# Optimization experiments

Measured on AMD Instinct MI355X. Metric: run time of the kernel, lower is better.

The kernel has to match this reference:

```python
import jax, jax.numpy as jnp
import numpy as np

N, E, D, L = 50000, 600000, 128, 3  # nodes, edges, feature dim, GIN layers
BN_EPS = 1e-5


def setup_inputs() -> dict:
    key = jax.random.key(0)
    ks = jax.random.split(key, 10)
    x = jax.random.normal(ks[0], (N, D), jnp.float32)
    edge_index = jax.random.randint(ks[1], (2, E), 0, N, jnp.int32)
    s = 1.0 / np.sqrt(D).astype(np.float32)
    W1 = jax.random.uniform(ks[2], (L, D, D), jnp.float32, -s, s)
    b1 = jax.random.uniform(ks[3], (L, D), jnp.float32, -s, s)
    W2 = jax.random.uniform(ks[4], (L, D, D), jnp.float32, -s, s)
    b2 = jax.random.uniform(ks[5], (L, D), jnp.float32, -s, s)
    gamma = jnp.ones((L, D), jnp.float32)
    beta = jnp.zeros((L, D), jnp.float32)
    fc_w = jax.random.uniform(ks[6], (D, 1), jnp.float32, -s, s)
    fc_b = jax.random.uniform(ks[7], (1,), jnp.float32, -s, s)
    return dict(x=x, edge_index=edge_index, W1=W1, b1=b1, W2=W2, b2=b2,
                gamma=gamma, beta=beta, fc_w=fc_w, fc_b=fc_b)


def reference(x, edge_index, W1, b1, W2, b2, gamma, beta, fc_w, fc_b):
    src, dst = edge_index[0], edge_index[1]
    h = x
    for l in range(L):
        # GINConv (eps=0): MLP(x_i + sum_{j->i} x_j)  -- gather then scatter-add
        agg = jax.ops.segment_sum(h[src], dst, num_segments=N)  # [N, D]
        z = h + agg
        z = jax.nn.relu(z @ W1[l] + b1[l]) @ W2[l] + b2[l]  # 2-layer MLP
        # BatchNorm1d (training mode: batch stats, biased variance)
        mu = z.mean(axis=0)
        var = z.var(axis=0)
        z = (z - mu) * jax.lax.rsqrt(var + BN_EPS) * gamma[l] + beta[l]
        h = jax.nn.relu(z)
    return h @ fc_w + fc_b  # [N, 1] per-node q-values
```

## Files before the change

kernel.cpp:

```cpp
#include <hip/hip_runtime.h>
#include <math.h>

#define NN 50000
#define NE 600000
#define DIM 128
#define LAYERS 3
#define BN_EPS 1e-5f

#define SC_ELE 2048
#define NSCAN ((NN + SC_ELE - 1) / SC_ELE)

__global__ void k_init(int* __restrict__ deg, float* __restrict__ bnstats) {
    int i = blockIdx.x * 256 + threadIdx.x;
    if (i < NN) deg[i] = 0;
    if (i < LAYERS * 2 * DIM) bnstats[i] = 0.0f;
}

__global__ void k_hist(const int* __restrict__ dst, int* __restrict__ deg) {
    int e = blockIdx.x * 256 + threadIdx.x;
    if (e < NE) atomicAdd(&deg[dst[e]], 1);
}

__global__ __launch_bounds__(1024) void k_scan1(const int* __restrict__ deg,
                                                int* __restrict__ part,
                                                int* __restrict__ bsum) {
    __shared__ int ws[16];
    const int t = threadIdx.x, lane = t & 63, wv = t >> 6;
    const int base = blockIdx.x * SC_ELE;
    const int e0 = base + 2 * t, e1 = e0 + 1;
    const int v0 = (e0 < NN) ? deg[e0] : 0;
    const int v1 = (e1 < NN) ? deg[e1] : 0;
    const int s = v0 + v1;
    int incl = s;
    #pragma unroll
    for (int o = 1; o < 64; o <<= 1) {
        int u = __shfl_up(incl, o);
        if (lane >= o) incl += u;
    }
    if (lane == 63) ws[wv] = incl;
    __syncthreads();
    if (wv == 0) {
        int x = (lane < 16) ? ws[lane] : 0;
        int ix = x;
        #pragma unroll
        for (int o = 1; o < 16; o <<= 1) {
            int u = __shfl_up(ix, o);
            if (lane >= o) ix += u;
        }
        if (lane < 16) ws[lane] = ix - x;
        if (lane == 15) bsum[blockIdx.x] = ix;
    }
    __syncthreads();
    const int excl = incl - s + ws[wv];
    if (e0 < NN) part[e0] = excl;
    if (e1 < NN) part[e1] = excl + v0;
}

__global__ void k_scan2(const int* __restrict__ bsum, int* __restrict__ boff) {
    const int lane = threadIdx.x;
    const int v = (lane < NSCAN) ? bsum[lane] : 0;
    int ix = v;
    #pragma unroll
    for (int o = 1; o < 64; o <<= 1) {
        int u = __shfl_up(ix, o);
        if (lane >= o) ix += u;
    }
    if (lane < NSCAN) boff[lane] = ix - v;
}

__global__ void k_scan3(const int* __restrict__ part, const int* __restrict__ boff,
                        int* __restrict__ off, int* __restrict__ cur) {
    int i = blockIdx.x * 256 + threadIdx.x;
    if (i < NN) {
        int o = part[i] + boff[i >> 11];
        off[i] = o;
        cur[i] = o;
        if (i == 0) off[NN] = NE;
    }
}

__global__ void k_fill(const int* __restrict__ src, const int* __restrict__ dst,
                       int* __restrict__ cur, int* __restrict__ csr) {
    int e = blockIdx.x * 256 + threadIdx.x;
    if (e < NE) {
        int p = atomicAdd(&cur[dst[e]], 1);
        csr[p] = src[e];
    }
}

__global__ __launch_bounds__(256) void k_agg(const float* __restrict__ h,
                                             const int* __restrict__ off,
                                             const int* __restrict__ csr,
                                             float* __restrict__ z) {
    int wid  = (blockIdx.x * 256 + threadIdx.x) >> 6;
    int lane = threadIdx.x & 63;
    if (wid >= NN) return;
    const int start = off[wid], end = off[wid + 1];
    float2 acc = *(const float2*)&h[(size_t)wid * DIM + lane * 2];
    int i = start;
    for (; i + 1 < end; i += 2) {
        int s0 = csr[i], s1 = csr[i + 1];
        float2 v0 = *(const float2*)&h[(size_t)s0 * DIM + lane * 2];
        float2 v1 = *(const float2*)&h[(size_t)s1 * DIM + lane * 2];
        acc.x += v0.x + v1.x;
        acc.y += v0.y + v1.y;
    }
    if (i < end) {
        int s0 = csr[i];
        float2 v0 = *(const float2*)&h[(size_t)s0 * DIM + lane * 2];
        acc.x += v0.x;
        acc.y += v0.y;
    }
    *(float2*)&z[(size_t)wid * DIM + lane * 2] = acc;
}

#define TM 32
__global__ __launch_bounds__(256, 2) void k_mlp(float* __restrict__ z,
                                                const float* __restrict__ W1,
                                                const float* __restrict__ b1,
                                                const float* __restrict__ W2,
                                                const float* __restrict__ b2,
                                                float* __restrict__ bnsum,
                                                float* __restrict__ bnsq) {
    __shared__ float zt[TM][DIM];
    __shared__ float w[DIM][DIM];
    const int t = threadIdx.x;
    const int c = t & 31;
    const int r = t >> 5;
    const int row0 = blockIdx.x * TM;

    #pragma unroll
    for (int i = 0; i < 4; ++i) {
        int f4 = t + i * 256;
        int rr = f4 >> 5, c4 = f4 & 31;
        int g  = row0 + rr;
        float4 v = make_float4(0.f, 0.f, 0.f, 0.f);
        if (g < NN) v = *(const float4*)&z[(size_t)g * DIM + c4 * 4];
        *(float4*)&zt[rr][c4 * 4] = v;
    }
    #pragma unroll
    for (int i = 0; i < 16; ++i) {
        int f4 = t + i * 256;
        int k = f4 >> 5, j4 = f4 & 31;
        *(float4*)&w[k][j4 * 4] = *(const float4*)&W1[k * DIM + j4 * 4];
    }
    __syncthreads();

    float acc[4][4];
    #pragma unroll
    for (int i = 0; i < 4; ++i)
        #pragma unroll
        for (int j = 0; j < 4; ++j) acc[i][j] = 0.0f;

    for (int k = 0; k < DIM; k += 4) {
        float4 a4[4];
        #pragma unroll
        for (int i = 0; i < 4; ++i) a4[i] = *(const float4*)&zt[r * 4 + i][k];
        #pragma unroll
        for (int kk = 0; kk < 4; ++kk) {
            const float4 b = *(const float4*)&w[k + kk][c * 4];
            #pragma unroll
            for (int i = 0; i < 4; ++i) {
                const float a = (&a4[i].x)[kk];
                acc[i][0] = fmaf(a, b.x, acc[i][0]);
                acc[i][1] = fmaf(a, b.y, acc[i][1]);
                acc[i][2] = fmaf(a, b.z, acc[i][2]);
                acc[i][3] = fmaf(a, b.w, acc[i][3]);
            }
        }
    }
    __syncthreads();

    const float4 bias1 = *(const float4*)&b1[c * 4];
    #pragma unroll
    for (int i = 0; i < 4; ++i) {
        float4 y;
        y.x = fmaxf(acc[i][0] + bias1.x, 0.f);
        y.y = fmaxf(acc[i][1] + bias1.y, 0.f);
        y.z = fmaxf(acc[i][2] + bias1.z, 0.f);
        y.w = fmaxf(acc[i][3] + bias1.w, 0.f);
        *(float4*)&zt[r * 4 + i][c * 4] = y;
    }
    #pragma unroll
    for (int i = 0; i < 16; ++i) {
        int f4 = t + i * 256;
        int k = f4 >> 5, j4 = f4 & 31;
        *(float4*)&w[k][j4 * 4] = *(const float4*)&W2[k * DIM + j4 * 4];
    }
    __syncthreads();

    #pragma unroll
    for (int i = 0; i < 4; ++i)
        #pragma unroll
        for (int j = 0; j < 4; ++j) acc[i][j] = 0.0f;

    for (int k = 0; k < DIM; k += 4) {
        float4 a4[4];
        #pragma unroll
        for (int i = 0; i < 4; ++i) a4[i] = *(const float4*)&zt[r * 4 + i][k];
        #pragma unroll
        for (int kk = 0; kk < 4; ++kk) {
            const float4 b = *(const float4*)&w[k + kk][c * 4];
            #pragma unroll
            for (int i = 0; i < 4; ++i) {
                const float a = (&a4[i].x)[kk];
                acc[i][0] = fmaf(a, b.x, acc[i][0]);
                acc[i][1] = fmaf(a, b.y, acc[i][1]);
                acc[i][2] = fmaf(a, b.z, acc[i][2]);
                acc[i][3] = fmaf(a, b.w, acc[i][3]);
            }
        }
    }
    __syncthreads();

    const float4 bias2 = *(const float4*)&b2[c * 4];
    float s[4] = {0.f, 0.f, 0.f, 0.f};
    float q[4] = {0.f, 0.f, 0.f, 0.f};
    #pragma unroll
    for (int i = 0; i < 4; ++i) {
        int g = row0 + r * 4 + i;
        float4 zv;
        zv.x = acc[i][0] + bias2.x;
        zv.y = acc[i][1] + bias2.y;
        zv.z = acc[i][2] + bias2.z;
        zv.w = acc[i][3] + bias2.w;
        if (g < NN) {
            *(float4*)&z[(size_t)g * DIM + c * 4] = zv;
            s[0] += zv.x; s[1] += zv.y; s[2] += zv.z; s[3] += zv.w;
            q[0] += zv.x * zv.x; q[1] += zv.y * zv.y;
            q[2] += zv.z * zv.z; q[3] += zv.w * zv.w;
        }
    }
    float* scratch = &zt[0][0];
    #pragma unroll
    for (int j = 0; j < 4; ++j) {
        scratch[r * DIM + c * 4 + j]        = s[j];
        scratch[1024 + r * DIM + c * 4 + j] = q[j];
    }
    __syncthreads();
    if (t < DIM) {
        float ss = 0.f, qq = 0.f;
        #pragma unroll
        for (int rr = 0; rr < 8; ++rr) {
            ss += scratch[rr * DIM + t];
            qq += scratch[1024 + rr * DIM + t];
        }
        atomicAdd(&bnsum[t], ss);
        atomicAdd(&bnsq[t], qq);
    }
}

__global__ __launch_bounds__(256) void k_norm(const float* __restrict__ z,
                                              const float* __restrict__ bnsum,
                                              const float* __restrict__ bnsq,
                                              const float* __restrict__ gamma,
                                              const float* __restrict__ beta,
                                              float* __restrict__ h) {
    int f4 = blockIdx.x * 256 + threadIdx.x;
    if (f4 >= NN * DIM / 4) return;
    int c0 = (f4 & 31) * 4;
    const float invN = 1.0f / (float)NN;
    float sc[4], sh[4];
    #pragma unroll
    for (int j = 0; j < 4; ++j) {
        int col = c0 + j;
        float mu  = bnsum[col] * invN;
        float var = bnsq[col] * invN - mu * mu;
        float k   = rsqrtf(var + BN_EPS) * gamma[col];
        sc[j] = k;
        sh[j] = beta[col] - mu * k;
    }
    float4 v = *(const float4*)&z[(size_t)f4 * 4];
    float4 o;
    o.x = fmaxf(fmaf(v.x, sc[0], sh[0]), 0.f);
    o.y = fmaxf(fmaf(v.y, sc[1], sh[1]), 0.f);
    o.z = fmaxf(fmaf(v.z, sc[2], sh[2]), 0.f);
    o.w = fmaxf(fmaf(v.w, sc[3], sh[3]), 0.f);
    *(float4*)&h[(size_t)f4 * 4] = o;
}

__global__ __launch_bounds__(256) void k_fc(const float* __restrict__ h,
                                            const float* __restrict__ fc_w,
                                            const float* __restrict__ fc_b,
                                            float* __restrict__ out) {
    int wid  = (blockIdx.x * 256 + threadIdx.x) >> 6;
    int lane = threadIdx.x & 63;
    if (wid >= NN) return;
    float2 v = *(const float2*)&h[(size_t)wid * DIM + lane * 2];
    float2 wv = *(const float2*)&fc_w[lane * 2];
    float s = v.x * wv.x + v.y * wv.y;
    #pragma unroll
    for (int o = 32; o >= 1; o >>= 1) s += __shfl_down(s, o);
    if (lane == 0) out[wid] = s + fc_b[0];
}

extern "C" void kernel_launch(void* const* d_in, const int* in_sizes, int n_in,
                              void* d_out, int out_size, void* d_ws, size_t ws_size,
                              hipStream_t stream) {
    const float* x     = (const float*)d_in[0];
    const int*   src   = (const int*)d_in[1];
    const int*   dst   = ((const int*)d_in[1]) + NE;
    const float* W1    = (const float*)d_in[2];
    const float* b1    = (const float*)d_in[3];
    const float* W2    = (const float*)d_in[4];
    const float* b2    = (const float*)d_in[5];
    const float* gamma = (const float*)d_in[6];
    const float* beta  = (const float*)d_in[7];
    const float* fc_w  = (const float*)d_in[8];
    const float* fc_b  = (const float*)d_in[9];
    float* out = (float*)d_out;

    char* ws = (char*)d_ws;
    size_t o = 0;
    auto carve = [&](size_t bytes) {
        char* p = ws + o;
        o += (bytes + 15) & ~(size_t)15;
        return p;
    };
    int*   deg     = (int*)carve(NN * 4);
    int*   off     = (int*)carve((NN + 1) * 4);
    int*   cur     = (int*)carve(NN * 4);
    int*   csr     = (int*)carve(NE * 4);
    int*   part    = (int*)carve(NN * 4);
    int*   bsum    = (int*)carve(NSCAN * 4);
    int*   boff    = (int*)carve(NSCAN * 4);
    float* bnstats = (float*)carve(LAYERS * 2 * DIM * 4);
    float* zbuf    = (float*)carve((size_t)NN * DIM * 4);
    float* h0      = (float*)carve((size_t)NN * DIM * 4);
    float* h1      = (float*)carve((size_t)NN * DIM * 4);

    k_init<<<(NN + 255) / 256, 256, 0, stream>>>(deg, bnstats);
    k_hist<<<(NE + 255) / 256, 256, 0, stream>>>(dst, deg);
    k_scan1<<<NSCAN, 1024, 0, stream>>>(deg, part, bsum);
    k_scan2<<<1, 64, 0, stream>>>(bsum, boff);
    k_scan3<<<(NN + 255) / 256, 256, 0, stream>>>(part, boff, off, cur);
    k_fill<<<(NE + 255) / 256, 256, 0, stream>>>(src, dst, cur, csr);

    const float* hin = x;
    float* hbuf[2] = {h0, h1};
    const int nblk_mlp  = (NN + TM - 1) / TM;
    const int nblk_agg  = (NN * 64 + 255) / 256;
    const int nblk_norm = (NN * DIM / 4 + 255) / 256;

    for (int l = 0; l < LAYERS; ++l) {
        float* hout = hbuf[l & 1];
        k_agg<<<nblk_agg, 256, 0, stream>>>(hin, off, csr, zbuf);
        k_mlp<<<nblk_mlp, 256, 0, stream>>>(zbuf,
                                            W1 + (size_t)l * DIM * DIM, b1 + l * DIM,
                                            W2 + (size_t)l * DIM * DIM, b2 + l * DIM,
                                            bnstats + l * DIM,
                                            bnstats + LAYERS * DIM + l * DIM);
        k_norm<<<nblk_norm, 256, 0, stream>>>(zbuf,
                                              bnstats + l * DIM,
                                              bnstats + LAYERS * DIM + l * DIM,
                                              gamma + l * DIM, beta + l * DIM, hout);
        hin = hout;
    }

    k_fc<<<(NN * 64 + 255) / 256, 256, 0, stream>>>(hin, fc_w, fc_b, out);
}
```

Measured before the change: 572.1 us.

## Fuse aggregation, MLP and deferred BatchNorm into one per-layer kernel

Merges the gather/scatter aggregation into the MLP kernel so aggregated rows go straight into shared memory instead of a global z buffer. BatchNorm+ReLU is applied on the fly when the next layer (or the final FC) reads neighbor rows, using per-column scale/shift from a tiny finalize kernel, which removes the separate normalize pass. Weights are now read from global/L1 instead of being staged in a 64KB LDS tile, allowing higher occupancy (launch bounds 4). The cost is redundant normalize math on every gathered row, and weight reads no longer staged in LDS may add memory pressure in the GEMM loops.

```diff
diff --git a/kernel.cpp b/kernel.cpp
--- a/kernel.cpp
+++ b/kernel.cpp
@@ -9,6 +9,7 @@
 
 #define SC_ELE 2048
 #define NSCAN ((NN + SC_ELE - 1) / SC_ELE)
+#define TM 32
 
 __global__ void k_init(int* __restrict__ deg, float* __restrict__ bnstats) {
     int i = blockIdx.x * 256 + threadIdx.x;
@@ -88,61 +89,79 @@
     }
 }
 
-__global__ __launch_bounds__(256) void k_agg(const float* __restrict__ h,
-                                             const int* __restrict__ off,
-                                             const int* __restrict__ csr,
-                                             float* __restrict__ z) {
-    int wid  = (blockIdx.x * 256 + threadIdx.x) >> 6;
-    int lane = threadIdx.x & 63;
-    if (wid >= NN) return;
-    const int start = off[wid], end = off[wid + 1];
-    float2 acc = *(const float2*)&h[(size_t)wid * DIM + lane * 2];
-    int i = start;
-    for (; i + 1 < end; i += 2) {
-        int s0 = csr[i], s1 = csr[i + 1];
-        float2 v0 = *(const float2*)&h[(size_t)s0 * DIM + lane * 2];
-        float2 v1 = *(const float2*)&h[(size_t)s1 * DIM + lane * 2];
-        acc.x += v0.x + v1.x;
-        acc.y += v0.y + v1.y;
-    }
-    if (i < end) {
-        int s0 = csr[i];
-        float2 v0 = *(const float2*)&h[(size_t)s0 * DIM + lane * 2];
-        acc.x += v0.x;
-        acc.y += v0.y;
-    }
-    *(float2*)&z[(size_t)wid * DIM + lane * 2] = acc;
-}
-
-#define TM 32
-__global__ __launch_bounds__(256, 2) void k_mlp(float* __restrict__ z,
-                                                const float* __restrict__ W1,
-                                                const float* __restrict__ b1,
-                                                const float* __restrict__ W2,
-                                                const float* __restrict__ b2,
-                                                float* __restrict__ bnsum,
-                                                float* __restrict__ bnsq) {
+__global__ void k_fin(const float* __restrict__ bnsum, const float* __restrict__ bnsq,
+                      const float* __restrict__ gamma, const float* __restrict__ beta,
+                      float* __restrict__ scsh) {
+    int j = threadIdx.x;
+    const float invN = 1.0f / (float)NN;
+    float mu  = bnsum[j] * invN;
+    float var = bnsq[j] * invN - mu * mu;
+    float k   = rsqrtf(var + BN_EPS) * gamma[j];
+    scsh[j]       = k;
+    scsh[DIM + j] = beta[j] - mu * k;
+}
+
+template <int NORM>
+__global__ __launch_bounds__(256, 4) void k_layer(
+        const float* __restrict__ hprev, const float* __restrict__ scsh,
+        const int* __restrict__ off, const int* __restrict__ csr,
+        const float* __restrict__ W1, const float* __restrict__ b1,
+        const float* __restrict__ W2, const float* __restrict__ b2,
+        float* __restrict__ zout,
+        float* __restrict__ bnsum, float* __restrict__ bnsq) {
     __shared__ float zt[TM][DIM];
-    __shared__ float w[DIM][DIM];
     const int t = threadIdx.x;
+    const int lane = t & 63, wv = t >> 6;
     const int c = t & 31;
     const int r = t >> 5;
     const int row0 = blockIdx.x * TM;
 
-    #pragma unroll
-    for (int i = 0; i < 4; ++i) {
-        int f4 = t + i * 256;
-        int rr = f4 >> 5, c4 = f4 & 31;
-        int g  = row0 + rr;
-        float4 v = make_float4(0.f, 0.f, 0.f, 0.f);
-        if (g < NN) v = *(const float4*)&z[(size_t)g * DIM + c4 * 4];
-        *(float4*)&zt[rr][c4 * 4] = v;
-    }
-    #pragma unroll
-    for (int i = 0; i < 16; ++i) {
-        int f4 = t + i * 256;
-        int k = f4 >> 5, j4 = f4 & 31;
-        *(float4*)&w[k][j4 * 4] = *(const float4*)&W1[k * DIM + j4 * 4];
+    {
+        float2 scv, shv;
+        if (NORM) {
+            scv = *(const float2*)&scsh[lane * 2];
+            shv = *(const float2*)&scsh[DIM + lane * 2];
+        }
+        #pragma unroll
+        for (int nb = 0; nb < 8; ++nb) {
+            const int row = wv * 8 + nb;
+            const int n = row0 + row;
+            float2 acc = make_float2(0.f, 0.f);
+            if (n < NN) {
+                float2 v = *(const float2*)&hprev[(size_t)n * DIM + lane * 2];
+                if (NORM) {
+                    v.x = fmaxf(fmaf(v.x, scv.x, shv.x), 0.f);
+                    v.y = fmaxf(fmaf(v.y, scv.y, shv.y), 0.f);
+                }
+                acc = v;
+                const int end = off[n + 1];
+                int i = off[n];
+                for (; i + 1 < end; i += 2) {
+                    int s0 = csr[i], s1 = csr[i + 1];
+                    float2 v0 = *(const float2*)&hprev[(size_t)s0 * DIM + lane * 2];
+                    float2 v1 = *(const float2*)&hprev[(size_t)s1 * DIM + lane * 2];
+                    if (NORM) {
+                        v0.x = fmaxf(fmaf(v0.x, scv.x, shv.x), 0.f);
+                        v0.y = fmaxf(fmaf(v0.y, scv.y, shv.y), 0.f);
+                        v1.x = fmaxf(fmaf(v1.x, scv.x, shv.x), 0.f);
+                        v1.y = fmaxf(fmaf(v1.y, scv.y, shv.y), 0.f);
+                    }
+                    acc.x += v0.x + v1.x;
+                    acc.y += v0.y + v1.y;
+                }
+                if (i < end) {
+                    int s0 = csr[i];
+                    float2 v0 = *(const float2*)&hprev[(size_t)s0 * DIM + lane * 2];
+                    if (NORM) {
+                        v0.x = fmaxf(fmaf(v0.x, scv.x, shv.x), 0.f);
+                        v0.y = fmaxf(fmaf(v0.y, scv.y, shv.y), 0.f);
+                    }
+                    acc.x += v0.x;
+                    acc.y += v0.y;
+                }
+            }
+            *(float2*)&zt[row][lane * 2] = acc;
+        }
     }
     __syncthreads();
 
@@ -158,7 +177,7 @@
         for (int i = 0; i < 4; ++i) a4[i] = *(const float4*)&zt[r * 4 + i][k];
         #pragma unroll
         for (int kk = 0; kk < 4; ++kk) {
-            const float4 b = *(const float4*)&w[k + kk][c * 4];
+            const float4 b = *(const float4*)&W1[(k + kk) * DIM + c * 4];
             #pragma unroll
             for (int i = 0; i < 4; ++i) {
                 const float a = (&a4[i].x)[kk];
@@ -181,12 +200,6 @@
         y.w = fmaxf(acc[i][3] + bias1.w, 0.f);
         *(float4*)&zt[r * 4 + i][c * 4] = y;
     }
-    #pragma unroll
-    for (int i = 0; i < 16; ++i) {
-        int f4 = t + i * 256;
-        int k = f4 >> 5, j4 = f4 & 31;
-        *(float4*)&w[k][j4 * 4] = *(const float4*)&W2[k * DIM + j4 * 4];
-    }
     __syncthreads();
 
     #pragma unroll
@@ -200,7 +213,7 @@
         for (int i = 0; i < 4; ++i) a4[i] = *(const float4*)&zt[r * 4 + i][k];
         #pragma unroll
         for (int kk = 0; kk < 4; ++kk) {
-            const float4 b = *(const float4*)&w[k + kk][c * 4];
+            const float4 b = *(const float4*)&W2[(k + kk) * DIM + c * 4];
             #pragma unroll
             for (int i = 0; i < 4; ++i) {
                 const float a = (&a4[i].x)[kk];
@@ -225,7 +238,7 @@
         zv.z = acc[i][2] + bias2.z;
         zv.w = acc[i][3] + bias2.w;
         if (g < NN) {
-            *(float4*)&z[(size_t)g * DIM + c * 4] = zv;
+            *(float4*)&zout[(size_t)g * DIM + c * 4] = zv;
             s[0] += zv.x; s[1] += zv.y; s[2] += zv.z; s[3] += zv.w;
             q[0] += zv.x * zv.x; q[1] += zv.y * zv.y;
             q[2] += zv.z * zv.z; q[3] += zv.w * zv.w;
@@ -250,43 +263,19 @@
     }
 }
 
-__global__ __launch_bounds__(256) void k_norm(const float* __restrict__ z,
-                                              const float* __restrict__ bnsum,
-                                              const float* __restrict__ bnsq,
-                                              const float* __restrict__ gamma,
-                                              const float* __restrict__ beta,
-                                              float* __restrict__ h) {
-    int f4 = blockIdx.x * 256 + threadIdx.x;
-    if (f4 >= NN * DIM / 4) return;
-    int c0 = (f4 & 31) * 4;
-    const float invN = 1.0f / (float)NN;
-    float sc[4], sh[4];
-    #pragma unroll
-    for (int j = 0; j < 4; ++j) {
-        int col = c0 + j;
-        float mu  = bnsum[col] * invN;
-        float var = bnsq[col] * invN - mu * mu;
-        float k   = rsqrtf(var + BN_EPS) * gamma[col];
-        sc[j] = k;
-        sh[j] = beta[col] - mu * k;
-    }
-    float4 v = *(const float4*)&z[(size_t)f4 * 4];
-    float4 o;
-    o.x = fmaxf(fmaf(v.x, sc[0], sh[0]), 0.f);
-    o.y = fmaxf(fmaf(v.y, sc[1], sh[1]), 0.f);
-    o.z = fmaxf(fmaf(v.z, sc[2], sh[2]), 0.f);
-    o.w = fmaxf(fmaf(v.w, sc[3], sh[3]), 0.f);
-    *(float4*)&h[(size_t)f4 * 4] = o;
-}
-
-__global__ __launch_bounds__(256) void k_fc(const float* __restrict__ h,
+__global__ __launch_bounds__(256) void k_fc(const float* __restrict__ z,
+                                            const float* __restrict__ scsh,
                                             const float* __restrict__ fc_w,
                                             const float* __restrict__ fc_b,
                                             float* __restrict__ out) {
     int wid  = (blockIdx.x * 256 + threadIdx.x) >> 6;
     int lane = threadIdx.x & 63;
     if (wid >= NN) return;
-    float2 v = *(const float2*)&h[(size_t)wid * DIM + lane * 2];
+    float2 v = *(const float2*)&z[(size_t)wid * DIM + lane * 2];
+    float2 scv = *(const float2*)&scsh[lane * 2];
+    float2 shv = *(const float2*)&scsh[DIM + lane * 2];
+    v.x = fmaxf(fmaf(v.x, scv.x, shv.x), 0.f);
+    v.y = fmaxf(fmaf(v.y, scv.y, shv.y), 0.f);
     float2 wv = *(const float2*)&fc_w[lane * 2];
     float s = v.x * wv.x + v.y * wv.y;
     #pragma unroll
@@ -325,9 +314,9 @@
     int*   bsum    = (int*)carve(NSCAN * 4);
     int*   boff    = (int*)carve(NSCAN * 4);
     float* bnstats = (float*)carve(LAYERS * 2 * DIM * 4);
-    float* zbuf    = (float*)carve((size_t)NN * DIM * 4);
-    float* h0      = (float*)carve((size_t)NN * DIM * 4);
-    float* h1      = (float*)carve((size_t)NN * DIM * 4);
+    float* scsh    = (float*)carve(LAYERS * 2 * DIM * 4);
+    float* zA      = (float*)carve((size_t)NN * DIM * 4);
+    float* zB      = (float*)carve((size_t)NN * DIM * 4);
 
     k_init<<<(NN + 255) / 256, 256, 0, stream>>>(deg, bnstats);
     k_hist<<<(NE + 255) / 256, 256, 0, stream>>>(dst, deg);
@@ -336,26 +325,27 @@
     k_scan3<<<(NN + 255) / 256, 256, 0, stream>>>(part, boff, off, cur);
     k_fill<<<(NE + 255) / 256, 256, 0, stream>>>(src, dst, cur, csr);
 
-    const float* hin = x;
-    float* hbuf[2] = {h0, h1};
-    const int nblk_mlp  = (NN + TM - 1) / TM;
-    const int nblk_agg  = (NN * 64 + 255) / 256;
-    const int nblk_norm = (NN * DIM / 4 + 255) / 256;
-
+    const int nblk = (NN + TM - 1) / TM;
+    float* zbuf[2] = {zA, zB};
     for (int l = 0; l < LAYERS; ++l) {
-        float* hout = hbuf[l & 1];
-        k_agg<<<nblk_agg, 256, 0, stream>>>(hin, off, csr, zbuf);
-        k_mlp<<<nblk_mlp, 256, 0, stream>>>(zbuf,
-                                            W1 + (size_t)l * DIM * DIM, b1 + l * DIM,
-                                            W2 + (size_t)l * DIM * DIM, b2 + l * DIM,
-                                            bnstats + l * DIM,
-                                            bnstats + LAYERS * DIM + l * DIM);
-        k_norm<<<nblk_norm, 256, 0, stream>>>(zbuf,
-                                              bnstats + l * DIM,
-                                              bnstats + LAYERS * DIM + l * DIM,
-                                              gamma + l * DIM, beta + l * DIM, hout);
-        hin = hout;
-    }
-
-    k_fc<<<(NN * 64 + 255) / 256, 256, 0, stream>>>(hin, fc_w, fc_b, out);
-}
+        const float* hin = (l == 0) ? x : zbuf[(l + 1) & 1];
+        float* zo = zbuf[l & 1];
+        float* sum_l = bnstats + l * DIM;
+        float* sq_l  = bnstats + LAYERS * DIM + l * DIM;
+        float* scsh_prev = scsh + (l - 1) * 2 * DIM;
+        if (l == 0)
+            k_layer<0><<<nblk, 256, 0, stream>>>(hin, nullptr, off, csr,
+                                                 W1, b1, W2, b2, zo, sum_l, sq_l);
+        else
+            k_layer<1><<<nblk, 256, 0, stream>>>(hin, scsh_prev, off, csr,
+                                                 W1 + (size_t)l * DIM * DIM, b1 + l * DIM,
+                                                 W2 + (size_t)l * DIM * DIM, b2 + l * DIM,
+                                                 zo, sum_l, sq_l);
+        k_fin<<<1, 128, 0, stream>>>(sum_l, sq_l, gamma + l * DIM, beta + l * DIM,
+                                     scsh + l * 2 * DIM);
+    }
+
+    k_fc<<<(NN * 64 + 255) / 256, 256, 0, stream>>>(zbuf[(LAYERS + 1) & 1],
+                                                    scsh + (LAYERS - 1) * 2 * DIM,
+                                                    fc_w, fc_b, out);
+}
```

New measurement: 642.5 us. 1.12x slower.
